# Performance work log

Hardware: AMD Instinct MI355X
Metric: run time of the kernel (lower is better)

The kernel has to match this reference:

```python
import jax, jax.numpy as jnp
import numpy as np

N_NODES = 50000
D_FEAT = 128
N_EDGES = 600000
HIDDEN_1 = 128
HIDDEN_2 = 64


def setup_inputs() -> dict:
    key = jax.random.key(0)
    ks = jax.random.split(key, 8)
    features = jax.random.normal(ks[0], (N_NODES, D_FEAT), dtype=jnp.float32)
    edges = jax.random.randint(ks[1], (N_EDGES, 2), 0, N_NODES, dtype=jnp.int64)
    s1 = 1.0 / np.sqrt(D_FEAT)
    s2 = 1.0 / np.sqrt(2 * HIDDEN_1)
    s3 = 1.0 / np.sqrt(HIDDEN_2)
    return {
        "features": features,
        "edges": edges,
        "W_nb": jax.random.normal(ks[2], (D_FEAT, HIDDEN_1), dtype=jnp.float32) * s1,
        "b_nb": jnp.zeros((HIDDEN_1,), dtype=jnp.float32),
        "W_self": jax.random.normal(ks[3], (D_FEAT, HIDDEN_1), dtype=jnp.float32) * s1,
        "b_self": jnp.zeros((HIDDEN_1,), dtype=jnp.float32),
        "W_att1": jax.random.normal(ks[4], (2 * HIDDEN_1, HIDDEN_2), dtype=jnp.float32) * s2,
        "b_att1": jnp.zeros((HIDDEN_2,), dtype=jnp.float32),
        "W_att2": jax.random.normal(ks[5], (HIDDEN_2, 1), dtype=jnp.float32) * s3,
        "b_att2": jnp.zeros((1,), dtype=jnp.float32),
    }


def reference(features, edges, W_nb, b_nb, W_self, b_self, W_att1, b_att1, W_att2, b_att2):
    # gather endpoint node features for each edge: [E, D_FEAT]
    f1 = features[edges[:, 0]]
    f2 = features[edges[:, 1]]
    # per-endpoint dense projections with relu (inference: no dropout)
    h1 = jax.nn.relu(f1 @ W_nb + b_nb)      # [E, H1]
    h2 = jax.nn.relu(f2 @ W_self + b_self)  # [E, H1]
    h = jnp.concatenate([h1, h2], axis=1)   # [E, 2*H1]
    h = jax.nn.relu(h @ W_att1 + b_att1)    # [E, H2]
    weight = h @ W_att2 + b_att2            # [E, 1], linear output
    return weight
```

## Files before the change

kernel.cpp:

```cpp
#include <hip/hip_runtime.h>


#define N_NODES 50000
#define D_FEAT  128
#define H1      128
#define H2      64
#define N_EDGES 600000

typedef unsigned short u16;
typedef __attribute__((ext_vector_type(8))) short bf16x8;
typedef __attribute__((ext_vector_type(4))) float f32x4;

union FragU { uint4 u; bf16x8 v; };

static __device__ __forceinline__ unsigned bfpack(float a, float b) {
    union { float f; unsigned u; } x, y; x.f = a; y.f = b;
    unsigned lo = (x.u + 0x7fffu + ((x.u >> 16) & 1u)) >> 16;
    unsigned hi = (y.u + 0x7fffu + ((y.u >> 16) & 1u)) & 0xffff0000u;
    return lo | hi;
}
static __device__ __forceinline__ u16 f2bf(float f) {
    union { float f; unsigned u; } v; v.f = f;
    return (u16)((v.u + 0x7fffu + ((v.u >> 16) & 1u)) >> 16);
}
static __device__ __forceinline__ float bflo(unsigned u) {
    union { unsigned u; float f; } v; v.u = u << 16; return v.f;
}
static __device__ __forceinline__ float bfhi(unsigned u) {
    union { unsigned u; float f; } v; v.u = u & 0xffff0000u; return v.f;
}

__global__ __launch_bounds__(256) void prep_kernel(
    const float* __restrict__ Wnb, const float* __restrict__ Wsf,
    const float* __restrict__ Wat1,
    u16* __restrict__ W1F, u16* __restrict__ W2F)
{
    const int t = threadIdx.x;
    const int b = blockIdx.x;
    if (b < 16) {
        const int cs = b;
        const int kc = t >> 6, q = (t >> 4) & 3, m = t & 15;
        const int col = cs * 16 + m;
        const float* src = (col < H1) ? (Wnb + col) : (Wsf + (col - H1));
        const int k0 = kc * 32 + q * 8;
        float e[8];
        #pragma unroll
        for (int j = 0; j < 8; ++j) e[j] = src[(size_t)(k0 + j) * H1];
        uint4 pk = make_uint4(bfpack(e[0], e[1]), bfpack(e[2], e[3]),
                              bfpack(e[4], e[5]), bfpack(e[6], e[7]));
        *((uint4*)&W1F[((cs * 4 + kc) * 64 + q * 16 + m) * 8]) = pk;
    } else {
        for (int i = t; i < 4 * 8 * 64; i += 256) {
            const int lane = i & 63, pair = i >> 6;
            const int kc = pair & 7, cs2 = pair >> 3;
            const int q = lane >> 4, m = lane & 15;
            const int col2 = cs2 * 16 + m;
            const int k0 = kc * 32 + q * 8;
            float e[8];
            #pragma unroll
            for (int j = 0; j < 8; ++j) e[j] = Wat1[(size_t)(k0 + j) * H2 + col2];
            uint4 pk = make_uint4(bfpack(e[0], e[1]), bfpack(e[2], e[3]),
                                  bfpack(e[4], e[5]), bfpack(e[6], e[7]));
            *((uint4*)&W2F[(pair * 64 + lane) * 8]) = pk;
        }
    }
}

__global__ __launch_bounds__(256) void node_kernel(
    const float* __restrict__ feat,
    const u16* __restrict__ W1F,  const u16* __restrict__ W2F,
    const float* __restrict__ bnb,  const float* __restrict__ bsf,
    const float* __restrict__ bat1,
    u16* __restrict__ a1, u16* __restrict__ a2)
{
    __shared__ u16 Abuf[4 * 4 * 64 * 8];
    __shared__ u16 Hbuf[4 * 8 * 64 * 8];

    const int t    = threadIdx.x;
    const int w    = t >> 6;
    const int lane = t & 63;
    const int m    = lane & 15;
    const int q    = lane >> 4;
    const int n0   = blockIdx.x * 64;

    FragU w1f[4][4];
    #pragma unroll
    for (int ms = 0; ms < 4; ++ms)
        #pragma unroll
        for (int kc = 0; kc < 4; ++kc)
            w1f[ms][kc].u = *((const uint4*)&W1F[(((w * 4 + ms) * 4 + kc) * 64 + lane) * 8]);

    #pragma unroll
    for (int s = 0; s < 8; ++s) {
        const int i   = s * 256 + t;
        const int row = i >> 5;
        const int c4  = i & 31;
        const int gn  = n0 + row;
        float4 v = make_float4(0.f, 0.f, 0.f, 0.f);
        if (gn < N_NODES)
            v = *((const float4*)(feat + (size_t)gn * D_FEAT + c4 * 4));
        const int k0  = c4 * 4;
        const int kc  = k0 >> 5;
        const int qq  = (k0 >> 3) & 3;
        const int j0  = k0 & 7;
        const int idx = (((row >> 4) * 4 + kc) * 64 + (qq * 16 + (row & 15))) * 8 + j0;
        uint2 p; p.x = bfpack(v.x, v.y); p.y = bfpack(v.z, v.w);
        *((uint2*)&Abuf[idx]) = p;
    }

    f32x4 acc1[4][4];
    #pragma unroll
    for (int i = 0; i < 4; ++i)
        #pragma unroll
        for (int j = 0; j < 4; ++j)
            acc1[i][j] = (f32x4){0.f, 0.f, 0.f, 0.f};

    __syncthreads();

    #pragma unroll
    for (int kc = 0; kc < 4; ++kc) {
        #pragma unroll
        for (int ns = 0; ns < 4; ++ns) {
            FragU ff; ff.u = *((const uint4*)&Abuf[((ns * 4 + kc) * 64 + lane) * 8]);
            #pragma unroll
            for (int ms = 0; ms < 4; ++ms)
                acc1[ms][ns] = __builtin_amdgcn_mfma_f32_16x16x32_bf16(
                    w1f[ms][kc].v, ff.v, acc1[ms][ns], 0, 0, 0);
        }
    }

    #pragma unroll
    for (int ms = 0; ms < 4; ++ms) {
        const int hcol0 = w * 64 + ms * 16 + q * 4;
        const float* bsrc = (hcol0 < H1) ? (bnb + hcol0) : (bsf + (hcol0 - H1));
        const float4 bb = *((const float4*)bsrc);
        const int kc2 = hcol0 >> 5;
        const int q2  = (hcol0 >> 3) & 3;
        const int j0  = hcol0 & 7;
        #pragma unroll
        for (int ns = 0; ns < 4; ++ns) {
            const f32x4 a = acc1[ms][ns];
            const float v0 = fmaxf(a.x + bb.x, 0.f);
            const float v1 = fmaxf(a.y + bb.y, 0.f);
            const float v2 = fmaxf(a.z + bb.z, 0.f);
            const float v3 = fmaxf(a.w + bb.w, 0.f);
            const int idx = ((ns * 8 + kc2) * 64 + (q2 * 16 + m)) * 8 + j0;
            uint2 p; p.x = bfpack(v0, v1); p.y = bfpack(v2, v3);
            *((uint2*)&Hbuf[idx]) = p;
        }
    }

    FragU w2f[2][4];
    #pragma unroll
    for (int ns2 = 0; ns2 < 2; ++ns2) {
        const int cs2 = (w & 1) * 2 + ns2;
        #pragma unroll
        for (int kcl = 0; kcl < 4; ++kcl) {
            const int kc = kcl + ((w < 2) ? 0 : 4);
            w2f[ns2][kcl].u = *((const uint4*)&W2F[((cs2 * 8 + kc) * 64 + lane) * 8]);
        }
    }

    f32x4 acc2[4][2];
    #pragma unroll
    for (int i = 0; i < 4; ++i) { acc2[i][0] = (f32x4){0.f,0.f,0.f,0.f};
                                  acc2[i][1] = (f32x4){0.f,0.f,0.f,0.f}; }

    __syncthreads();

    #pragma unroll
    for (int kcl = 0; kcl < 4; ++kcl) {
        const int kc2 = kcl + ((w < 2) ? 0 : 4);
        #pragma unroll
        for (int ms = 0; ms < 4; ++ms) {
            FragU hf; hf.u = *((const uint4*)&Hbuf[((ms * 8 + kc2) * 64 + lane) * 8]);
            #pragma unroll
            for (int ns2 = 0; ns2 < 2; ++ns2)
                acc2[ms][ns2] = __builtin_amdgcn_mfma_f32_16x16x32_bf16(
                    w2f[ns2][kcl].v, hf.v, acc2[ms][ns2], 0, 0, 0);
        }
    }

    u16* aout = (w < 2) ? a1 : a2;
    const int colbase = (w & 1) * 32;
    #pragma unroll
    for (int ns2 = 0; ns2 < 2; ++ns2) {
        const int c0 = colbase + ns2 * 16 + q * 4;
        float4 b2 = make_float4(0.f, 0.f, 0.f, 0.f);
        if (w < 2) b2 = *((const float4*)(bat1 + c0));
        #pragma unroll
        for (int ms = 0; ms < 4; ++ms) {
            const int node = n0 + ms * 16 + m;
            if (node < N_NODES) {
                const f32x4 a = acc2[ms][ns2];
                ushort4 pk;
                pk.x = f2bf(a.x + b2.x); pk.y = f2bf(a.y + b2.y);
                pk.z = f2bf(a.z + b2.z); pk.w = f2bf(a.w + b2.w);
                *((ushort4*)(aout + (size_t)node * H2 + c0)) = pk;
            }
        }
    }
}

static __device__ __forceinline__ float edot(uint4 q1, uint4 q2,
                                             float4 w0, float4 w1) {
    float s = 0.f;
    s += fmaxf(bflo(q1.x) + bflo(q2.x), 0.f) * w0.x;
    s += fmaxf(bfhi(q1.x) + bfhi(q2.x), 0.f) * w0.y;
    s += fmaxf(bflo(q1.y) + bflo(q2.y), 0.f) * w0.z;
    s += fmaxf(bfhi(q1.y) + bfhi(q2.y), 0.f) * w0.w;
    s += fmaxf(bflo(q1.z) + bflo(q2.z), 0.f) * w1.x;
    s += fmaxf(bfhi(q1.z) + bfhi(q2.z), 0.f) * w1.y;
    s += fmaxf(bflo(q1.w) + bflo(q2.w), 0.f) * w1.z;
    s += fmaxf(bfhi(q1.w) + bfhi(q2.w), 0.f) * w1.w;
    return s;
}

__global__ __launch_bounds__(256) void edge_kernel(
    const int* __restrict__ edges,
    const u16* __restrict__ a1, const u16* __restrict__ a2,
    const float* __restrict__ Wat2, const float* __restrict__ bat2,
    float* __restrict__ out)
{
    const int t = threadIdx.x;
    const int l = t & 7;
    const int g = t >> 3;
    const int base = blockIdx.x * 128 + g;

    const float4 w0 = ((const float4*)Wat2)[l * 2 + 0];
    const float4 w1 = ((const float4*)Wat2)[l * 2 + 1];
    const float  bias = bat2[0];

    int  e[4]; bool v[4]; int2 ep[4];
    #pragma unroll
    for (int i = 0; i < 4; ++i) {
        e[i] = base + i * 32;
        v[i] = e[i] < N_EDGES;
        ep[i] = v[i] ? ((const int2*)edges)[e[i]] : make_int2(0, 0);
    }

    uint4 q1[4], q2[4];
    #pragma unroll
    for (int i = 0; i < 4; ++i) {
        q1[i] = ((const uint4*)(a1 + (size_t)ep[i].x * H2))[l];
        q2[i] = ((const uint4*)(a2 + (size_t)ep[i].y * H2))[l];
    }

    float s[4];
    #pragma unroll
    for (int i = 0; i < 4; ++i) {
        s[i] = edot(q1[i], q2[i], w0, w1);
        s[i] += __shfl_down(s[i], 4, 8);
        s[i] += __shfl_down(s[i], 2, 8);
        s[i] += __shfl_down(s[i], 1, 8);
    }

    if (l == 0) {
        #pragma unroll
        for (int i = 0; i < 4; ++i)
            if (v[i]) out[e[i]] = s[i] + bias;
    }
}

extern "C" void kernel_launch(void* const* d_in, const int* in_sizes, int n_in,
                              void* d_out, int out_size, void* d_ws, size_t ws_size,
                              hipStream_t stream) {
    const float* feat  = (const float*)d_in[0];
    const int*   edges = (const int*)d_in[1];
    const float* Wnb   = (const float*)d_in[2];
    const float* bnb   = (const float*)d_in[3];
    const float* Wsf   = (const float*)d_in[4];
    const float* bsf   = (const float*)d_in[5];
    const float* Wat1  = (const float*)d_in[6];
    const float* bat1  = (const float*)d_in[7];
    const float* Wat2  = (const float*)d_in[8];
    const float* bat2  = (const float*)d_in[9];
    float* out = (float*)d_out;

    u16* a1  = (u16*)d_ws;
    u16* a2  = a1 + (size_t)N_NODES * H2;
    u16* W1F = a2 + (size_t)N_NODES * H2;
    u16* W2F = W1F + 16 * 4 * 64 * 8;

    prep_kernel<<<17, 256, 0, stream>>>(Wnb, Wsf, Wat1, W1F, W2F);

    const int node_blocks = (N_NODES + 63) / 64;
    node_kernel<<<node_blocks, 256, 0, stream>>>(feat, W1F, W2F,
                                                 bnb, bsf, bat1, a1, a2);

    const int edge_blocks = (N_EDGES + 127) / 128;
    edge_kernel<<<edge_blocks, 256, 0, stream>>>(edges, a1, a2, Wat2, bat2, out);
}
```

Measured before the change: 125.8 us.

## Switch intermediate precision from bf16 to fp16 with packed half math in edge dot

Replaces the bf16 storage and MFMA ops with fp16 throughout. Conversions now use hardware float-to-half instead of manual bit-rounding, the edge kernel's add and relu run as packed half2 ops, and the node feature staging loads two float4 per lane straight into fragment order. The aim is to cut ALU work in conversion and in the per-edge combine, and to simplify the shared-memory staging. The cost is fp16's narrower range, which could overflow or lose precision compared with bf16 for large activations.

```diff
diff --git a/kernel.cpp b/kernel.cpp
--- a/kernel.cpp
+++ b/kernel.cpp
@@ -8,26 +8,20 @@
 #define N_EDGES 600000
 
 typedef unsigned short u16;
-typedef __attribute__((ext_vector_type(8))) short bf16x8;
+typedef _Float16 f16;
+typedef __attribute__((ext_vector_type(8))) _Float16 f16x8;
+typedef __attribute__((ext_vector_type(2))) _Float16 f16x2;
+typedef __attribute__((ext_vector_type(2))) float f32x2;
 typedef __attribute__((ext_vector_type(4))) float f32x4;
 
-union FragU { uint4 u; bf16x8 v; };
-
-static __device__ __forceinline__ unsigned bfpack(float a, float b) {
-    union { float f; unsigned u; } x, y; x.f = a; y.f = b;
-    unsigned lo = (x.u + 0x7fffu + ((x.u >> 16) & 1u)) >> 16;
-    unsigned hi = (y.u + 0x7fffu + ((y.u >> 16) & 1u)) & 0xffff0000u;
-    return lo | hi;
-}
-static __device__ __forceinline__ u16 f2bf(float f) {
-    union { float f; unsigned u; } v; v.f = f;
-    return (u16)((v.u + 0x7fffu + ((v.u >> 16) & 1u)) >> 16);
-}
-static __device__ __forceinline__ float bflo(unsigned u) {
-    union { unsigned u; float f; } v; v.u = u << 16; return v.f;
-}
-static __device__ __forceinline__ float bfhi(unsigned u) {
-    union { unsigned u; float f; } v; v.u = u & 0xffff0000u; return v.f;
+union FragH { uint4 u; f16x8 v; };
+union H2U   { unsigned u; f16x2 h; };
+
+static __device__ __forceinline__ u16 f2h(float f) {
+    union { f16 h; u16 u; } v; v.h = (f16)f; return v.u;
+}
+static __device__ __forceinline__ unsigned hpack(float a, float b) {
+    return (unsigned)f2h(a) | ((unsigned)f2h(b) << 16);
 }
 
 __global__ __launch_bounds__(256) void prep_kernel(
@@ -46,21 +40,21 @@
         float e[8];
         #pragma unroll
         for (int j = 0; j < 8; ++j) e[j] = src[(size_t)(k0 + j) * H1];
-        uint4 pk = make_uint4(bfpack(e[0], e[1]), bfpack(e[2], e[3]),
-                              bfpack(e[4], e[5]), bfpack(e[6], e[7]));
+        uint4 pk = make_uint4(hpack(e[0], e[1]), hpack(e[2], e[3]),
+                              hpack(e[4], e[5]), hpack(e[6], e[7]));
         *((uint4*)&W1F[((cs * 4 + kc) * 64 + q * 16 + m) * 8]) = pk;
     } else {
         for (int i = t; i < 4 * 8 * 64; i += 256) {
             const int lane = i & 63, pair = i >> 6;
-            const int kc = pair & 7, cs2 = pair >> 3;
             const int q = lane >> 4, m = lane & 15;
+            const int cs2 = pair >> 3, kc = pair & 7;
             const int col2 = cs2 * 16 + m;
             const int k0 = kc * 32 + q * 8;
             float e[8];
             #pragma unroll
             for (int j = 0; j < 8; ++j) e[j] = Wat1[(size_t)(k0 + j) * H2 + col2];
-            uint4 pk = make_uint4(bfpack(e[0], e[1]), bfpack(e[2], e[3]),
-                                  bfpack(e[4], e[5]), bfpack(e[6], e[7]));
+            uint4 pk = make_uint4(hpack(e[0], e[1]), hpack(e[2], e[3]),
+                                  hpack(e[4], e[5]), hpack(e[6], e[7]));
             *((uint4*)&W2F[(pair * 64 + lane) * 8]) = pk;
         }
     }
@@ -83,31 +77,31 @@
     const int q    = lane >> 4;
     const int n0   = blockIdx.x * 64;
 
-    FragU w1f[4][4];
+    {
+        const int kcs = t >> 6;
+        const int k0  = kcs * 32 + q * 8;
+        #pragma unroll
+        for (int it = 0; it < 4; ++it) {
+            const int gn = n0 + it * 16 + m;
+            float4 va = make_float4(0.f,0.f,0.f,0.f), vb = va;
+            if (gn < N_NODES) {
+                const float* src = feat + (size_t)gn * D_FEAT + k0;
+                va = *((const float4*)src);
+                vb = *((const float4*)(src + 4));
+            }
+            uint4 pk = make_uint4(hpack(va.x, va.y), hpack(va.z, va.w),
+                                  hpack(vb.x, vb.y), hpack(vb.z, vb.w));
+            *((uint4*)&Abuf[(((it * 4 + kcs) * 64) + (t & 63)) * 8]) = pk;
+        }
+    }
+
+    FragH w1f[4][4];
     #pragma unroll
     for (int ms = 0; ms < 4; ++ms)
         #pragma unroll
         for (int kc = 0; kc < 4; ++kc)
             w1f[ms][kc].u = *((const uint4*)&W1F[(((w * 4 + ms) * 4 + kc) * 64 + lane) * 8]);
 
-    #pragma unroll
-    for (int s = 0; s < 8; ++s) {
-        const int i   = s * 256 + t;
-        const int row = i >> 5;
-        const int c4  = i & 31;
-        const int gn  = n0 + row;
-        float4 v = make_float4(0.f, 0.f, 0.f, 0.f);
-        if (gn < N_NODES)
-            v = *((const float4*)(feat + (size_t)gn * D_FEAT + c4 * 4));
-        const int k0  = c4 * 4;
-        const int kc  = k0 >> 5;
-        const int qq  = (k0 >> 3) & 3;
-        const int j0  = k0 & 7;
-        const int idx = (((row >> 4) * 4 + kc) * 64 + (qq * 16 + (row & 15))) * 8 + j0;
-        uint2 p; p.x = bfpack(v.x, v.y); p.y = bfpack(v.z, v.w);
-        *((uint2*)&Abuf[idx]) = p;
-    }
-
     f32x4 acc1[4][4];
     #pragma unroll
     for (int i = 0; i < 4; ++i)
@@ -121,10 +115,10 @@
     for (int kc = 0; kc < 4; ++kc) {
         #pragma unroll
         for (int ns = 0; ns < 4; ++ns) {
-            FragU ff; ff.u = *((const uint4*)&Abuf[((ns * 4 + kc) * 64 + lane) * 8]);
+            FragH ff; ff.u = *((const uint4*)&Abuf[((ns * 4 + kc) * 64 + lane) * 8]);
             #pragma unroll
             for (int ms = 0; ms < 4; ++ms)
-                acc1[ms][ns] = __builtin_amdgcn_mfma_f32_16x16x32_bf16(
+                acc1[ms][ns] = __builtin_amdgcn_mfma_f32_16x16x32_f16(
                     w1f[ms][kc].v, ff.v, acc1[ms][ns], 0, 0, 0);
         }
     }
@@ -145,12 +139,12 @@
             const float v2 = fmaxf(a.z + bb.z, 0.f);
             const float v3 = fmaxf(a.w + bb.w, 0.f);
             const int idx = ((ns * 8 + kc2) * 64 + (q2 * 16 + m)) * 8 + j0;
-            uint2 p; p.x = bfpack(v0, v1); p.y = bfpack(v2, v3);
+            uint2 p; p.x = hpack(v0, v1); p.y = hpack(v2, v3);
             *((uint2*)&Hbuf[idx]) = p;
         }
     }
 
-    FragU w2f[2][4];
+    FragH w2f[2][4];
     #pragma unroll
     for (int ns2 = 0; ns2 < 2; ++ns2) {
         const int cs2 = (w & 1) * 2 + ns2;
@@ -173,10 +167,10 @@
         const int kc2 = kcl + ((w < 2) ? 0 : 4);
         #pragma unroll
         for (int ms = 0; ms < 4; ++ms) {
-            FragU hf; hf.u = *((const uint4*)&Hbuf[((ms * 8 + kc2) * 64 + lane) * 8]);
+            FragH hf; hf.u = *((const uint4*)&Hbuf[((ms * 8 + kc2) * 64 + lane) * 8]);
             #pragma unroll
             for (int ns2 = 0; ns2 < 2; ++ns2)
-                acc2[ms][ns2] = __builtin_amdgcn_mfma_f32_16x16x32_bf16(
+                acc2[ms][ns2] = __builtin_amdgcn_mfma_f32_16x16x32_f16(
                     w2f[ns2][kcl].v, hf.v, acc2[ms][ns2], 0, 0, 0);
         }
     }
@@ -194,25 +188,42 @@
             if (node < N_NODES) {
                 const f32x4 a = acc2[ms][ns2];
                 ushort4 pk;
-                pk.x = f2bf(a.x + b2.x); pk.y = f2bf(a.y + b2.y);
-                pk.z = f2bf(a.z + b2.z); pk.w = f2bf(a.w + b2.w);
+                pk.x = f2h(a.x + b2.x); pk.y = f2h(a.y + b2.y);
+                pk.z = f2h(a.z + b2.z); pk.w = f2h(a.w + b2.w);
                 *((ushort4*)(aout + (size_t)node * H2 + c0)) = pk;
             }
         }
     }
 }
 
-static __device__ __forceinline__ float edot(uint4 q1, uint4 q2,
+static __device__ __forceinline__ float edot(uint4 a, uint4 b,
                                              float4 w0, float4 w1) {
+    const f16x2 z = (f16x2)(f16)0;
     float s = 0.f;
-    s += fmaxf(bflo(q1.x) + bflo(q2.x), 0.f) * w0.x;
-    s += fmaxf(bfhi(q1.x) + bfhi(q2.x), 0.f) * w0.y;
-    s += fmaxf(bflo(q1.y) + bflo(q2.y), 0.f) * w0.z;
-    s += fmaxf(bfhi(q1.y) + bfhi(q2.y), 0.f) * w0.w;
-    s += fmaxf(bflo(q1.z) + bflo(q2.z), 0.f) * w1.x;
-    s += fmaxf(bfhi(q1.z) + bfhi(q2.z), 0.f) * w1.y;
-    s += fmaxf(bflo(q1.w) + bflo(q2.w), 0.f) * w1.z;
-    s += fmaxf(bfhi(q1.w) + bfhi(q2.w), 0.f) * w1.w;
+    {
+        H2U x, y; x.u = a.x; y.u = b.x;
+        f16x2 r = __builtin_elementwise_max(x.h + y.h, z);
+        f32x2 f = __builtin_convertvector(r, f32x2);
+        s = fmaf(f.x, w0.x, fmaf(f.y, w0.y, s));
+    }
+    {
+        H2U x, y; x.u = a.y; y.u = b.y;
+        f16x2 r = __builtin_elementwise_max(x.h + y.h, z);
+        f32x2 f = __builtin_convertvector(r, f32x2);
+        s = fmaf(f.x, w0.z, fmaf(f.y, w0.w, s));
+    }
+    {
+        H2U x, y; x.u = a.z; y.u = b.z;
+        f16x2 r = __builtin_elementwise_max(x.h + y.h, z);
+        f32x2 f = __builtin_convertvector(r, f32x2);
+        s = fmaf(f.x, w1.x, fmaf(f.y, w1.y, s));
+    }
+    {
+        H2U x, y; x.u = a.w; y.u = b.w;
+        f16x2 r = __builtin_elementwise_max(x.h + y.h, z);
+        f32x2 f = __builtin_convertvector(r, f32x2);
+        s = fmaf(f.x, w1.z, fmaf(f.y, w1.w, s));
+    }
     return s;
 }
 
```

Result: no change. 123.4 us (-1.9%).
